# Kernel optimization log

Measured on AMD Instinct MI355X. Metric: run time of the kernel, lower is better.

The kernel has to match this reference:

```python
import jax, jax.numpy as jnp
import numpy as np

H = 1024
V = 50000
L = 2048


def setup_inputs() -> dict:
    key = jax.random.key(0)
    ks = jax.random.split(key, 16)
    s = 0.02  # weight init scale
    return {
        "input_tok": jax.random.randint(ks[0], (1,), 0, V, dtype=jnp.int64),
        "h0": jax.random.normal(ks[1], (1, 1, H), jnp.float32),
        "c0": jax.random.normal(ks[2], (1, 1, H), jnp.float32),
        "encoder_outputs": jax.random.normal(ks[3], (L, H), jnp.float32),
        "emb": jax.random.normal(ks[4], (V, H), jnp.float32) * s,
        "attn_W": jax.random.normal(ks[5], (H, H), jnp.float32) * s,
        "attn_b": jax.random.normal(ks[6], (H,), jnp.float32) * s,
        "comb_W": jax.random.normal(ks[7], (H, 2 * H), jnp.float32) * s,
        "comb_b": jax.random.normal(ks[8], (H,), jnp.float32) * s,
        "W_ih": jax.random.normal(ks[9], (4 * H, H), jnp.float32) * s,
        "W_hh": jax.random.normal(ks[10], (4 * H, H), jnp.float32) * s,
        "b_ih": jax.random.normal(ks[11], (4 * H,), jnp.float32) * s,
        "b_hh": jax.random.normal(ks[12], (4 * H,), jnp.float32) * s,
        "out_W": jax.random.normal(ks[13], (V, H), jnp.float32) * s,
        "out_b": jax.random.normal(ks[14], (V,), jnp.float32) * s,
    }


def reference(input_tok, h0, c0, encoder_outputs, emb, attn_W, attn_b,
              comb_W, comb_b, W_ih, W_hh, b_ih, b_hh, out_W, out_b):
    # embedded: [1, H] (single decode token; view(-1) in the source forces input_len == 1)
    e = emb[input_tok][0]  # [H]

    # attention branch (note: in the original module this result is dead code --
    # the loop below overwrites `output` -- but we compute it faithfully)
    scores = encoder_outputs @ (attn_W @ e + attn_b)        # [L]
    a = jax.nn.softmax(scores)                               # [L]
    ctx = a @ encoder_outputs                                # [H]
    combined = jnp.tanh(comb_W @ jnp.concatenate([e, ctx]) + comb_b)  # [H] (unused)

    # single LSTM cell step (torch gate order: i, f, g, o)
    h, c = h0[0, 0], c0[0, 0]                                # [H], [H]
    gates = W_ih @ e + b_ih + W_hh @ h + b_hh                # [4H]
    i, f, g, o = jnp.split(gates, 4)
    i, f, o = jax.nn.sigmoid(i), jax.nn.sigmoid(f), jax.nn.sigmoid(o)
    g = jnp.tanh(g)
    c_new = f * c + i * g
    h_new = o * jnp.tanh(c_new)

    # output projection + log_softmax over vocab
    logits = h_new @ out_W.T + out_b                         # [V]
    log_probs = jax.nn.log_softmax(logits)[None, :]          # [1, V]
    return log_probs, h_new[None, None, :], c_new[None, None, :]
```

## Files before the change

kernel.cpp:

```cpp
#include <hip/hip_runtime.h>
#include <math.h>

#define HH 1024
#define VV 50000
#define NB2 1250

__device__ __forceinline__ float wredsum(float v) {
#pragma unroll
    for (int o = 32; o > 0; o >>= 1) v += __shfl_xor(v, o);
    return v;
}

__global__ __launch_bounds__(256) void lstm_kernel(
    const int* __restrict__ tok, const float* __restrict__ emb,
    const float* __restrict__ h0, const float* __restrict__ c0,
    const float* __restrict__ W_ih, const float* __restrict__ W_hh,
    const float* __restrict__ b_ih, const float* __restrict__ b_hh,
    float* __restrict__ out)
{
    __shared__ float sg[4];
    const int g    = threadIdx.x >> 6;
    const int lane = threadIdx.x & 63;
    const int j    = blockIdx.x;
    const int t    = tok[0];
    const float* e = emb + (size_t)t * HH;

    const float* wi = W_ih + (size_t)(g * HH + j) * HH;
    const float* wh = W_hh + (size_t)(g * HH + j) * HH;

    float acc = 0.f;
#pragma unroll
    for (int k = 0; k < 4; ++k) {
        const int idx = k * 256 + lane * 4;
        const float4 a  = *(const float4*)(wi + idx);
        const float4 b  = *(const float4*)(wh + idx);
        const float4 ev = *(const float4*)(e  + idx);
        const float4 hv = *(const float4*)(h0 + idx);
        acc += a.x * ev.x + a.y * ev.y + a.z * ev.z + a.w * ev.w;
        acc += b.x * hv.x + b.y * hv.y + b.z * hv.z + b.w * hv.w;
    }
    acc = wredsum(acc);
    if (lane == 0) sg[g] = acc + b_ih[g * HH + j] + b_hh[g * HH + j];
    __syncthreads();

    if (threadIdx.x == 0) {
        const float si = 1.f / (1.f + expf(-sg[0]));
        const float sf = 1.f / (1.f + expf(-sg[1]));
        const float gg = tanhf(sg[2]);
        const float so = 1.f / (1.f + expf(-sg[3]));
        const float cn = sf * c0[j] + si * gg;
        const float hn = so * tanhf(cn);
        out[VV + j]      = hn;
        out[VV + HH + j] = cn;
    }
}

__global__ __launch_bounds__(256) void logits_kernel(
    const float* __restrict__ out_W, const float* __restrict__ out_b,
    const float* __restrict__ h,
    float* __restrict__ logits,
    float2* __restrict__ part)
{
    __shared__ float2 sp[4];
    const int wid  = threadIdx.x >> 6;
    const int lane = threadIdx.x & 63;
    const int gw   = blockIdx.x * 4 + wid;

    float4 hv[4];
#pragma unroll
    for (int k = 0; k < 4; ++k)
        hv[k] = *(const float4*)(h + k * 256 + lane * 4);

    float m = -INFINITY, s = 0.f;
#pragma unroll
    for (int i = 0; i < 5; ++i) {
        const int r0 = gw + (2 * i)     * 5000;
        const int r1 = gw + (2 * i + 1) * 5000;
        const float* w0 = out_W + (size_t)r0 * HH;
        const float* w1 = out_W + (size_t)r1 * HH;
        float a0 = 0.f, a1 = 0.f;
#pragma unroll
        for (int k = 0; k < 4; ++k) {
            const int idx = k * 256 + lane * 4;
            const float4 x0 = *(const float4*)(w0 + idx);
            const float4 x1 = *(const float4*)(w1 + idx);
            a0 += x0.x * hv[k].x + x0.y * hv[k].y + x0.z * hv[k].z + x0.w * hv[k].w;
            a1 += x1.x * hv[k].x + x1.y * hv[k].y + x1.z * hv[k].z + x1.w * hv[k].w;
        }
        const float v0 = wredsum(a0) + out_b[r0];
        const float v1 = wredsum(a1) + out_b[r1];
        if (lane == 0) { logits[r0] = v0; logits[r1] = v1; }
        const float nm = fmaxf(m, fmaxf(v0, v1));
        s = s * expf(m - nm) + expf(v0 - nm) + expf(v1 - nm);
        m = nm;
    }
    if (lane == 0) sp[wid] = make_float2(m, s);
    __syncthreads();
    if (threadIdx.x == 0) {
        float2 p = sp[0];
#pragma unroll
        for (int w = 1; w < 4; ++w) {
            const float2 q = sp[w];
            const float nm = fmaxf(p.x, q.x);
            p.y = p.y * expf(p.x - nm) + q.y * expf(q.x - nm);
            p.x = nm;
        }
        part[blockIdx.x] = p;
    }
}

__global__ __launch_bounds__(256) void logz_kernel(
    const float2* __restrict__ part, int nblk, float* __restrict__ logz)
{
    __shared__ float2 red[256];
    float m = -INFINITY, s = 0.f;
    for (int i = threadIdx.x; i < nblk; i += 256) {
        const float2 q = part[i];
        const float nm = fmaxf(m, q.x);
        s = s * expf(m - nm) + q.y * expf(q.x - nm);
        m = nm;
    }
    red[threadIdx.x] = make_float2(m, s);
    __syncthreads();
    for (int st = 128; st > 0; st >>= 1) {
        if (threadIdx.x < st) {
            float2 p = red[threadIdx.x], q = red[threadIdx.x + st];
            const float nm = fmaxf(p.x, q.x);
            p.y = p.y * expf(p.x - nm) + q.y * expf(q.x - nm);
            p.x = nm;
            red[threadIdx.x] = p;
        }
        __syncthreads();
    }
    if (threadIdx.x == 0) *logz = red[0].x + logf(red[0].y);
}

__global__ __launch_bounds__(256) void sub_kernel(
    float* __restrict__ logits, const float* __restrict__ logz)
{
    const float lz = *logz;
    const int v = blockIdx.x * 256 + threadIdx.x;
    if (v < VV) logits[v] -= lz;
}

extern "C" void kernel_launch(void* const* d_in, const int* in_sizes, int n_in,
                              void* d_out, int out_size, void* d_ws, size_t ws_size,
                              hipStream_t stream) {
    const int*   tok   = (const int*)  d_in[0];
    const float* h0    = (const float*)d_in[1];
    const float* c0    = (const float*)d_in[2];
    const float* emb   = (const float*)d_in[4];
    const float* W_ih  = (const float*)d_in[9];
    const float* W_hh  = (const float*)d_in[10];
    const float* b_ih  = (const float*)d_in[11];
    const float* b_hh  = (const float*)d_in[12];
    const float* out_W = (const float*)d_in[13];
    const float* out_b = (const float*)d_in[14];

    float* out = (float*)d_out;

    float2* part = (float2*)d_ws;
    float*  logz = (float*)(part + NB2);

    lstm_kernel<<<1024, 256, 0, stream>>>(tok, emb, h0, c0, W_ih, W_hh, b_ih, b_hh, out);
    logits_kernel<<<NB2, 256, 0, stream>>>(out_W, out_b, out + VV, out, part);
    logz_kernel<<<1, 256, 0, stream>>>(part, NB2, logz);
    sub_kernel<<<(VV + 255) / 256, 256, 0, stream>>>(out, logz);
}
```

Before: 416.2 us.

## Fuse logZ reduction into logits kernel and batch row loads with nontemporal reads

The logits kernel now issues all ten row loads per wave up front and reduces them together, which raises memory-level parallelism. Weight reads use nontemporal loads. A last-block ticket (reset in the LSTM kernel) replaces the separate logZ kernel, and the subtract kernel is vectorized to float4. Together these cut one launch and aim to improve bandwidth use on the ~200MB weight stream, at the cost of more registers and atomic/fence synchronization.

Result: slower. 452.3 us (+8.7%).

```diff
diff --git a/kernel.cpp b/kernel.cpp
--- a/kernel.cpp
+++ b/kernel.cpp
@@ -4,6 +4,12 @@
 #define HH 1024
 #define VV 50000
 #define NB2 1250
+
+typedef float f4 __attribute__((ext_vector_type(4)));
+
+__device__ __forceinline__ float dot4(f4 a, f4 b) {
+    return a.x * b.x + a.y * b.y + a.z * b.z + a.w * b.w;
+}
 
 __device__ __forceinline__ float wredsum(float v) {
 #pragma unroll
@@ -16,8 +22,11 @@
     const float* __restrict__ h0, const float* __restrict__ c0,
     const float* __restrict__ W_ih, const float* __restrict__ W_hh,
     const float* __restrict__ b_ih, const float* __restrict__ b_hh,
-    float* __restrict__ out)
+    float* __restrict__ out,
+    int* __restrict__ ticket)
 {
+    if (blockIdx.x == 0 && threadIdx.x == 0) *ticket = 0;
+
     __shared__ float sg[4];
     const int g    = threadIdx.x >> 6;
     const int lane = threadIdx.x & 63;
@@ -32,12 +41,12 @@
 #pragma unroll
     for (int k = 0; k < 4; ++k) {
         const int idx = k * 256 + lane * 4;
-        const float4 a  = *(const float4*)(wi + idx);
-        const float4 b  = *(const float4*)(wh + idx);
-        const float4 ev = *(const float4*)(e  + idx);
-        const float4 hv = *(const float4*)(h0 + idx);
-        acc += a.x * ev.x + a.y * ev.y + a.z * ev.z + a.w * ev.w;
-        acc += b.x * hv.x + b.y * hv.y + b.z * hv.z + b.w * hv.w;
+        const f4 a  = __builtin_nontemporal_load((const f4*)(wi + idx));
+        const f4 b  = __builtin_nontemporal_load((const f4*)(wh + idx));
+        const f4 ev = *(const f4*)(e  + idx);
+        const f4 hv = *(const f4*)(h0 + idx);
+        acc += dot4(a, ev);
+        acc += dot4(b, hv);
     }
     acc = wredsum(acc);
     if (lane == 0) sg[g] = acc + b_ih[g * HH + j] + b_hh[g * HH + j];
@@ -59,41 +68,54 @@
     const float* __restrict__ out_W, const float* __restrict__ out_b,
     const float* __restrict__ h,
     float* __restrict__ logits,
-    float2* __restrict__ part)
+    float2* __restrict__ part,
+    int* __restrict__ ticket,
+    float* __restrict__ logz)
 {
     __shared__ float2 sp[4];
+    __shared__ int slast;
     const int wid  = threadIdx.x >> 6;
     const int lane = threadIdx.x & 63;
     const int gw   = blockIdx.x * 4 + wid;
 
-    float4 hv[4];
+    f4 hv[4];
 #pragma unroll
     for (int k = 0; k < 4; ++k)
-        hv[k] = *(const float4*)(h + k * 256 + lane * 4);
+        hv[k] = *(const f4*)(h + k * 256 + lane * 4);
 
-    float m = -INFINITY, s = 0.f;
+    float acc[10];
 #pragma unroll
-    for (int i = 0; i < 5; ++i) {
-        const int r0 = gw + (2 * i)     * 5000;
-        const int r1 = gw + (2 * i + 1) * 5000;
-        const float* w0 = out_W + (size_t)r0 * HH;
-        const float* w1 = out_W + (size_t)r1 * HH;
-        float a0 = 0.f, a1 = 0.f;
+    for (int i = 0; i < 10; ++i) {
+        const float* w = out_W + (size_t)(gw + i * 5000) * HH;
+        float a = 0.f;
 #pragma unroll
         for (int k = 0; k < 4; ++k) {
-            const int idx = k * 256 + lane * 4;
-            const float4 x0 = *(const float4*)(w0 + idx);
-            const float4 x1 = *(const float4*)(w1 + idx);
-            a0 += x0.x * hv[k].x + x0.y * hv[k].y + x0.z * hv[k].z + x0.w * hv[k].w;
-            a1 += x1.x * hv[k].x + x1.y * hv[k].y + x1.z * hv[k].z + x1.w * hv[k].w;
+            const f4 x = __builtin_nontemporal_load((const f4*)(w + k * 256) + lane);
+            a += dot4(x, hv[k]);
         }
-        const float v0 = wredsum(a0) + out_b[r0];
-        const float v1 = wredsum(a1) + out_b[r1];
-        if (lane == 0) { logits[r0] = v0; logits[r1] = v1; }
-        const float nm = fmaxf(m, fmaxf(v0, v1));
-        s = s * expf(m - nm) + expf(v0 - nm) + expf(v1 - nm);
-        m = nm;
+        acc[i] = a;
     }
+
+#pragma unroll
+    for (int o = 32; o > 0; o >>= 1) {
+#pragma unroll
+        for (int i = 0; i < 10; ++i) acc[i] += __shfl_xor(acc[i], o);
+    }
+
+    float m = -INFINITY;
+#pragma unroll
+    for (int i = 0; i < 10; ++i) {
+        acc[i] += out_b[gw + i * 5000];
+        m = fmaxf(m, acc[i]);
+    }
+    if (lane == 0) {
+#pragma unroll
+        for (int i = 0; i < 10; ++i) logits[gw + i * 5000] = acc[i];
+    }
+    float s = 0.f;
+#pragma unroll
+    for (int i = 0; i < 10; ++i) s += expf(acc[i] - m);
+
     if (lane == 0) sp[wid] = make_float2(m, s);
     __syncthreads();
     if (threadIdx.x == 0) {
@@ -106,21 +128,22 @@
             p.x = nm;
         }
         part[blockIdx.x] = p;
+        __threadfence();
+        slast = (atomicAdd(ticket, 1) == NB2 - 1) ? 1 : 0;
     }
-}
+    __syncthreads();
+    if (!slast) return;
 
-__global__ __launch_bounds__(256) void logz_kernel(
-    const float2* __restrict__ part, int nblk, float* __restrict__ logz)
-{
+    __threadfence();
     __shared__ float2 red[256];
-    float m = -INFINITY, s = 0.f;
-    for (int i = threadIdx.x; i < nblk; i += 256) {
+    float mm = -INFINITY, ss = 0.f;
+    for (int i = threadIdx.x; i < NB2; i += 256) {
         const float2 q = part[i];
-        const float nm = fmaxf(m, q.x);
-        s = s * expf(m - nm) + q.y * expf(q.x - nm);
-        m = nm;
+        const float nm = fmaxf(mm, q.x);
+        ss = ss * expf(mm - nm) + q.y * expf(q.x - nm);
+        mm = nm;
     }
-    red[threadIdx.x] = make_float2(m, s);
+    red[threadIdx.x] = make_float2(mm, ss);
     __syncthreads();
     for (int st = 128; st > 0; st >>= 1) {
         if (threadIdx.x < st) {
@@ -136,11 +159,15 @@
 }
 
 __global__ __launch_bounds__(256) void sub_kernel(
-    float* __restrict__ logits, const float* __restrict__ logz)
+    f4* __restrict__ logits, const float* __restrict__ logz)
 {
     const float lz = *logz;
     const int v = blockIdx.x * 256 + threadIdx.x;
-    if (v < VV) logits[v] -= lz;
+    if (v < VV / 4) {
+        f4 t = logits[v];
+        t.x -= lz; t.y -= lz; t.z -= lz; t.w -= lz;
+        logits[v] = t;
+    }
 }
 
 extern "C" void kernel_launch(void* const* d_in, const int* in_sizes, int n_in,
@@ -159,11 +186,13 @@
 
     float* out = (float*)d_out;
 
-    float2* part = (float2*)d_ws;
-    float*  logz = (float*)(part + NB2);
+    float2* part   = (float2*)d_ws;
+    float*  logz   = (float*)(part + NB2);
+    int*    ticket = (int*)(logz + 1);
 
-    lstm_kernel<<<1024, 256, 0, stream>>>(tok, emb, h0, c0, W_ih, W_hh, b_ih, b_hh, out);
-    logits_kernel<<<NB2, 256, 0, stream>>>(out_W, out_b, out + VV, out, part);
-    logz_kernel<<<1, 256, 0, stream>>>(part, NB2, logz);
-    sub_kernel<<<(VV + 255) / 256, 256, 0, stream>>>(out, logz);
+    lstm_kernel<<<1024, 256, 0, stream>>>(tok, emb, h0, c0, W_ih, W_hh, b_ih, b_hh,
+                                          out, ticket);
+    logits_kernel<<<NB2, 256, 0, stream>>>(out_W, out_b, out + VV, out, part,
+                                           ticket, logz);
+    sub_kernel<<<(VV / 4 + 255) / 256, 256, 0, stream>>>((f4*)out, logz);
 }
```

## Fuse logZ reduction into subtract kernel and restructure logits row mapping

Applied to the files above, without the earlier changes.

Each wave in the logits kernel now handles four contiguous vocab rows with four independent accumulators and batched shuffles, replacing the strided ten-row loop with a running softmax. Grid size grows to 3125 blocks for more parallelism. The separate logZ and subtract kernels are merged: every block redundantly reduces the 3125 partials and then applies a vectorized subtract, removing one launch at the cost of duplicated reduction work across 49 blocks.

After: 414.4 us. About the same (-0.4%).

```diff
diff --git a/kernel.cpp b/kernel.cpp
--- a/kernel.cpp
+++ b/kernel.cpp
@@ -3,12 +3,12 @@
 
 #define HH 1024
 #define VV 50000
-#define NB2 1250
+#define NB2 3125
 
-__device__ __forceinline__ float wredsum(float v) {
-#pragma unroll
-    for (int o = 32; o > 0; o >>= 1) v += __shfl_xor(v, o);
-    return v;
+typedef float f4 __attribute__((ext_vector_type(4)));
+
+__device__ __forceinline__ float dot4(f4 a, f4 b) {
+    return a.x * b.x + a.y * b.y + a.z * b.z + a.w * b.w;
 }
 
 __global__ __launch_bounds__(256) void lstm_kernel(
@@ -32,14 +32,15 @@
 #pragma unroll
     for (int k = 0; k < 4; ++k) {
         const int idx = k * 256 + lane * 4;
-        const float4 a  = *(const float4*)(wi + idx);
-        const float4 b  = *(const float4*)(wh + idx);
-        const float4 ev = *(const float4*)(e  + idx);
-        const float4 hv = *(const float4*)(h0 + idx);
-        acc += a.x * ev.x + a.y * ev.y + a.z * ev.z + a.w * ev.w;
-        acc += b.x * hv.x + b.y * hv.y + b.z * hv.z + b.w * hv.w;
+        const f4 a  = *(const f4*)(wi + idx);
+        const f4 b  = *(const f4*)(wh + idx);
+        const f4 ev = *(const f4*)(e  + idx);
+        const f4 hv = *(const f4*)(h0 + idx);
+        acc += dot4(a, ev);
+        acc += dot4(b, hv);
     }
-    acc = wredsum(acc);
+#pragma unroll
+    for (int o = 32; o > 0; o >>= 1) acc += __shfl_xor(acc, o);
     if (lane == 0) sg[g] = acc + b_ih[g * HH + j] + b_hh[g * HH + j];
     __syncthreads();
 
@@ -65,35 +66,41 @@
     const int wid  = threadIdx.x >> 6;
     const int lane = threadIdx.x & 63;
     const int gw   = blockIdx.x * 4 + wid;
+    const int r0   = gw * 4;
 
-    float4 hv[4];
+    f4 hv[4];
 #pragma unroll
     for (int k = 0; k < 4; ++k)
-        hv[k] = *(const float4*)(h + k * 256 + lane * 4);
+        hv[k] = *(const f4*)(h + k * 256 + lane * 4);
 
-    float m = -INFINITY, s = 0.f;
+    float acc[4];
 #pragma unroll
-    for (int i = 0; i < 5; ++i) {
-        const int r0 = gw + (2 * i)     * 5000;
-        const int r1 = gw + (2 * i + 1) * 5000;
-        const float* w0 = out_W + (size_t)r0 * HH;
-        const float* w1 = out_W + (size_t)r1 * HH;
-        float a0 = 0.f, a1 = 0.f;
+    for (int j = 0; j < 4; ++j) {
+        const f4* w = (const f4*)(out_W + (size_t)(r0 + j) * HH);
+        const f4 x0 = w[lane];
+        const f4 x1 = w[lane + 64];
+        const f4 x2 = w[lane + 128];
+        const f4 x3 = w[lane + 192];
+        acc[j] = (dot4(x0, hv[0]) + dot4(x1, hv[1]))
+               + (dot4(x2, hv[2]) + dot4(x3, hv[3]));
+    }
+
 #pragma unroll
-        for (int k = 0; k < 4; ++k) {
-            const int idx = k * 256 + lane * 4;
-            const float4 x0 = *(const float4*)(w0 + idx);
-            const float4 x1 = *(const float4*)(w1 + idx);
-            a0 += x0.x * hv[k].x + x0.y * hv[k].y + x0.z * hv[k].z + x0.w * hv[k].w;
-            a1 += x1.x * hv[k].x + x1.y * hv[k].y + x1.z * hv[k].z + x1.w * hv[k].w;
-        }
-        const float v0 = wredsum(a0) + out_b[r0];
-        const float v1 = wredsum(a1) + out_b[r1];
-        if (lane == 0) { logits[r0] = v0; logits[r1] = v1; }
-        const float nm = fmaxf(m, fmaxf(v0, v1));
-        s = s * expf(m - nm) + expf(v0 - nm) + expf(v1 - nm);
-        m = nm;
+    for (int o = 32; o > 0; o >>= 1) {
+#pragma unroll
+        for (int j = 0; j < 4; ++j) acc[j] += __shfl_xor(acc[j], o);
     }
+
+    const f4 vb = *(const f4*)(out_b + r0);
+    acc[0] += vb.x; acc[1] += vb.y; acc[2] += vb.z; acc[3] += vb.w;
+    if (lane == 0) {
+        f4 st; st.x = acc[0]; st.y = acc[1]; st.z = acc[2]; st.w = acc[3];
+        *(f4*)(logits + r0) = st;
+    }
+    const float m = fmaxf(fmaxf(acc[0], acc[1]), fmaxf(acc[2], acc[3]));
+    const float s = expf(acc[0] - m) + expf(acc[1] - m)
+                  + expf(acc[2] - m) + expf(acc[3] - m);
+
     if (lane == 0) sp[wid] = make_float2(m, s);
     __syncthreads();
     if (threadIdx.x == 0) {
@@ -109,12 +116,12 @@
     }
 }
 
-__global__ __launch_bounds__(256) void logz_kernel(
-    const float2* __restrict__ part, int nblk, float* __restrict__ logz)
+__global__ __launch_bounds__(256) void logz_sub_kernel(
+    const float2* __restrict__ part, f4* __restrict__ logits)
 {
     __shared__ float2 red[256];
     float m = -INFINITY, s = 0.f;
-    for (int i = threadIdx.x; i < nblk; i += 256) {
+    for (int i = threadIdx.x; i < NB2; i += 256) {
         const float2 q = part[i];
         const float nm = fmaxf(m, q.x);
         s = s * expf(m - nm) + q.y * expf(q.x - nm);
@@ -132,15 +139,14 @@
         }
         __syncthreads();
     }
-    if (threadIdx.x == 0) *logz = red[0].x + logf(red[0].y);
-}
+    const float lz = red[0].x + logf(red[0].y);
 
-__global__ __launch_bounds__(256) void sub_kernel(
-    float* __restrict__ logits, const float* __restrict__ logz)
-{
-    const float lz = *logz;
     const int v = blockIdx.x * 256 + threadIdx.x;
-    if (v < VV) logits[v] -= lz;
+    if (v < VV / 4) {
+        f4 t = logits[v];
+        t.x -= lz; t.y -= lz; t.z -= lz; t.w -= lz;
+        logits[v] = t;
+    }
 }
 
 extern "C" void kernel_launch(void* const* d_in, const int* in_sizes, int n_in,
@@ -160,10 +166,9 @@
     float* out = (float*)d_out;
 
     float2* part = (float2*)d_ws;
-    float*  logz = (float*)(part + NB2);
 
-    lstm_kernel<<<1024, 256, 0, stream>>>(tok, emb, h0, c0, W_ih, W_hh, b_ih, b_hh, out);
+    lstm_kernel<<<1024, 256, 0, stream>>>(tok, emb, h0, c0, W_ih, W_hh,
+                                          b_ih, b_hh, out);
     logits_kernel<<<NB2, 256, 0, stream>>>(out_W, out_b, out + VV, out, part);
-    logz_kernel<<<1, 256, 0, stream>>>(part, NB2, logz);
-    sub_kernel<<<(VV + 255) / 256, 256, 0, stream>>>(out, logz);
+    logz_sub_kernel<<<(VV / 4 + 255) / 256, 256, 0, stream>>>(part, (f4*)out);
 }
```
